# Performance work log

Measured on AMD Instinct MI355X. Metric: run time of the kernel, lower is better.

The kernel has to match this reference:

```python
import itertools
import jax, jax.numpy as jnp
import numpy as np

N, C, D, S = 512, 128, 16, 10  # atoms, channels, irreps dim (0e+1o+2e+3o), species
IR_DIMS = {'0e': 1, '1o': 3}
MULS = {'0e': (23, 4, 1), '1o': (33, 6, 1)}  # path multiplicities for orders (3, 2, 1)


def _make_u(key, order, mul, ir_dim):
    # Synthetic stand-in for e3nn.reduced_symmetric_tensor_product_basis:
    # under permutation of the `order` leading D axes.
    shape = (D,) * order + (mul, ir_dim)
    u = jax.random.normal(key, shape, dtype=jnp.float32)
    mask = jax.random.bernoulli(jax.random.fold_in(key, 1), 0.1, shape)
    u = jnp.where(mask, u, 0.0)
    perms = list(itertools.permutations(range(order)))
    u = sum(jnp.transpose(u, p + (order, order + 1)) for p in perms) / len(perms)
    return u


def setup_inputs() -> dict:
    key = jax.random.key(0)
    ks = jax.random.split(key, 16)
    inp = {
        'x': jax.random.normal(ks[0], (N, C, D), dtype=jnp.float32),
        'index': jax.random.randint(ks[1], (N,), 0, S, dtype=jnp.int32),
    }
    i = 2
    for ir in IR_DIMS:
        for order, mul in zip((3, 2, 1), MULS[ir]):
            inp[f'u{order}_{ir}'] = _make_u(ks[i], order, mul, IR_DIMS[ir]); i += 1
            # gradient_normalization='element' -> init stddev mul**-0.5, no runtime scale
            inp[f'w{order}_{ir}'] = (jax.random.normal(ks[i], (S, mul, C), dtype=jnp.float32)
                                     * mul ** -0.5); i += 1
    return inp


def _contract(x, idx, u3, u2, u1, w3, w2, w1):
    # x: (N,C,D); uK: (D,)*K + (mulK, ir); wK: (S, mulK, C)
    w3i, w2i, w1i = w3[idx], w2[idx], w1[idx]  # species gather -> (N, mulK, C)
    # order 3: einsum('...jki,kc,cj->c...i', u3, w3i, x) batched over atoms.
    # Form p[n,c,k,j] = w3i[n,k,c]*x[n,c,j] first (small), then one big contraction.
    p = jnp.einsum('nkc,ncj->nckj', w3i, x)              # (N,C,mul3,D)
    out = jnp.einsum('abjki,nckj->ncabi', u3, p)         # (N,C,D,D,ir)
    # order 2: accumulate U2.w2, then contract one D axis with x
    out = out + jnp.einsum('abki,nkc->ncabi', u2, w2i)   # (N,C,D,D,ir)
    out = jnp.einsum('ncaji,ncj->ncai', out, x)          # (N,C,D,ir)
    # order 1: accumulate U1.w1, then final contraction with x
    out = out + jnp.einsum('aki,nkc->ncai', u1, w1i)     # (N,C,D,ir)
    out = jnp.einsum('ncji,ncj->nci', out, x)            # (N,C,ir)
    return out


def reference(x, index, u3_0e, w3_0e, u2_0e, w2_0e, u1_0e, w1_0e,
              u3_1o, w3_1o, u2_1o, w2_1o, u1_1o, w1_1o):
    out0 = _contract(x, index, u3_0e, u2_0e, u1_0e, w3_0e, w2_0e, w1_0e)  # (N,C,1)
    out1 = _contract(x, index, u3_1o, u2_1o, u1_1o, w3_1o, w2_1o, w1_1o)  # (N,C,3)
    return jnp.concatenate([out0, out1], axis=-1)  # (N,C,4) irreps 0e+1o
```

## Files before the change

kernel.cpp:

```cpp
#include <hip/hip_runtime.h>
#include <hip/hip_fp16.h>


#define DD     16
#define NATOM  512
#define NCH    128
#define NSPEC  10
#define NTP    1024
#define ATB    8
#define APT    2
#define MAXB   74
#define CHUNKS 8
#define NTC    128
#define TILE   8
#define NTILES (NTC / TILE)
#define CHALF  2
#define CT     8

#define WS_DESC  0
#define WS_ORDER 1024
#define WS_COEF  8192
#define COEF_BYTES (NSPEC * 2 * NTP * 64 * 4 * 2)
#define WS_PART  (WS_COEF + COEF_BYTES)

struct TermTable { unsigned v[NTP]; };
constexpr TermTable build_terms() {
  TermTable T{};
  int t = 0;
  for (int a = 0; a < DD; a++)
    for (int b = a; b < DD; b++)
      for (int j = b; j < DD; j++) {
        unsigned m = (a == b && b == j) ? 1u : ((a == b || b == j) ? 3u : 6u);
        T.v[t++] = (unsigned)(a | (b << 5) | (j << 10) | (3u << 15) | (m << 18));
      }
  for (int a = 0; a < DD; a++)
    for (int b = a; b < DD; b++) {
      unsigned m = (a == b) ? 1u : 2u;
      T.v[t++] = (unsigned)(a | (b << 5) | (16 << 10) | (2u << 15) | (m << 18));
    }
  for (int a = 0; a < DD; a++)
    T.v[t++] = (unsigned)(a | (16 << 5) | (16 << 10) | (1u << 15) | (1u << 18));
  while (t < NTP) T.v[t++] = (unsigned)(17 | (17 << 5) | (17 << 10));
  return T;
}
constexpr TermTable TERMS = build_terms();

__device__ void do_setup(const int* __restrict__ index, int* __restrict__ desc,
                         int* __restrict__ order) {
  __shared__ int cnt[NSPEC], cursor[NSPEC], bbase[NSPEC + 1];
  const int tid = threadIdx.x;
  if (tid < NSPEC) { cnt[tid] = 0; cursor[tid] = 0; }
  __syncthreads();
  for (int i = tid; i < NATOM; i += 128) atomicAdd(&cnt[index[i]], 1);
  for (int i = tid; i < MAXB * ATB; i += 128) order[i] = -1;
  __syncthreads();
  if (tid == 0) {
    int base = 0;
    for (int s = 0; s < NSPEC; s++) { bbase[s] = base; base += (cnt[s] + ATB - 1) / ATB; }
    bbase[NSPEC] = base;
  }
  __syncthreads();
  for (int i = tid; i < NATOM; i += 128) {
    int s = index[i];
    int pos = atomicAdd(&cursor[s], 1);
    order[bbase[s] * ATB + pos] = i;
  }
  for (int i = tid; i < MAXB; i += 128) {
    int sp = -1;
    for (int s = 0; s < NSPEC; s++)
      if (i >= bbase[s] && i < bbase[s + 1]) sp = s;
    desc[i] = sp;
  }
}

__global__ __launch_bounds__(128) void coef_setup_kernel(
    const float* __restrict__ u3_0, const float* __restrict__ w3_0,
    const float* __restrict__ u2_0, const float* __restrict__ w2_0,
    const float* __restrict__ u1_0, const float* __restrict__ w1_0,
    const float* __restrict__ u3_1, const float* __restrict__ w3_1,
    const float* __restrict__ u2_1, const float* __restrict__ w2_1,
    const float* __restrict__ u1_1, const float* __restrict__ w1_1,
    const int* __restrict__ index, int* __restrict__ desc,
    int* __restrict__ order, __half* __restrict__ coefh) {
  if (blockIdx.y == NTP / CT) {
    if (blockIdx.x == 0) do_setup(index, desc, order);
    return;
  }
  const int s = blockIdx.x;
  const int c = threadIdx.x;
  const int tbase = blockIdx.y * CT;

  __shared__ float us0[CT][23];
  __shared__ float us1[CT][99];

  for (int i = 0; i < CT; ++i) {
    const unsigned ev = TERMS.v[tbase + i];
    const int kind = (ev >> 15) & 7;
    const int a = ev & 31, b = (ev >> 5) & 31, j = (ev >> 10) & 31;
    if (kind == 3) {
      const int off = (a * DD + b) * DD + j;
      if (c < 23) us0[i][c] = u3_0[off * 23 + c];
      else if (c < 122) us1[i][c - 23] = u3_1[(size_t)off * 99 + (c - 23)];
    } else if (kind == 2) {
      const int off = a * DD + b;
      if (c < 4) us0[i][c] = u2_0[off * 4 + c];
      else if (c < 22) us1[i][c - 4] = u2_1[off * 18 + (c - 4)];
    } else if (kind == 1) {
      if (c < 1) us0[i][0] = u1_0[a];
      else if (c < 4) us1[i][c - 1] = u1_1[a * 3 + (c - 1)];
    }
  }
  __syncthreads();

  float r3_0[23], r3_1[33], r2_0[4], r2_1[6];
#pragma unroll
  for (int k = 0; k < 23; k++) r3_0[k] = w3_0[(s * 23 + k) * NCH + c];
#pragma unroll
  for (int k = 0; k < 33; k++) r3_1[k] = w3_1[(s * 33 + k) * NCH + c];
#pragma unroll
  for (int k = 0; k < 4; k++) r2_0[k] = w2_0[(s * 4 + k) * NCH + c];
#pragma unroll
  for (int k = 0; k < 6; k++) r2_1[k] = w2_1[(s * 6 + k) * NCH + c];
  const float r1_0 = w1_0[s * NCH + c];
  const float r1_1 = w1_1[s * NCH + c];

  for (int i = 0; i < CT; ++i) {
    const unsigned ev = TERMS.v[tbase + i];
    const int kind = (ev >> 15) & 7;
    const float fm = (float)((ev >> 18) & 7);
    float s0 = 0.f, s1 = 0.f, s2 = 0.f, s3 = 0.f;
    if (kind == 3) {
#pragma unroll
      for (int k = 0; k < 23; k++) s0 += us0[i][k] * r3_0[k];
#pragma unroll
      for (int k = 0; k < 33; k++) {
        const float w = r3_1[k];
        s1 += us1[i][k * 3 + 0] * w;
        s2 += us1[i][k * 3 + 1] * w;
        s3 += us1[i][k * 3 + 2] * w;
      }
    } else if (kind == 2) {
#pragma unroll
      for (int k = 0; k < 4; k++) s0 += us0[i][k] * r2_0[k];
#pragma unroll
      for (int k = 0; k < 6; k++) {
        const float w = r2_1[k];
        s1 += us1[i][k * 3 + 0] * w;
        s2 += us1[i][k * 3 + 1] * w;
        s3 += us1[i][k * 3 + 2] * w;
      }
    } else if (kind == 1) {
      s0 = us0[i][0] * r1_0;
      s1 = us1[i][0] * r1_1;
      s2 = us1[i][1] * r1_1;
      s3 = us1[i][2] * r1_1;
    }
    union { __half2 h2[2]; uint2 u; } pk;
    pk.h2[0] = __floats2half2_rn(fm * s0, fm * s1);
    pk.h2[1] = __floats2half2_rn(fm * s2, fm * s3);
    const size_t off =
        (((size_t)(s * 2 + (c >> 6)) * NTP + (tbase + i)) * 64 + (c & 63));
    *(uint2*)((char*)coefh + off * 8) = pk.u;
  }
}

__device__ __forceinline__ void stage_tile(const unsigned* __restrict__ gbase,
                                           int t0_tile, float* dst_base,
                                           int wave, int lane) {
  const unsigned* g = gbase + (size_t)(t0_tile + 2 * wave) * 128 + lane * 4;
  __builtin_amdgcn_global_load_lds(
      (const __attribute__((address_space(1))) unsigned int*)g,
      (__attribute__((address_space(3))) unsigned int*)(dst_base + wave * 256),
      16, 0, 0);
}

template <int CH>
__device__ __forceinline__ void eval_chunk(const unsigned* __restrict__ gbase,
                                           float (*lbuf)[TILE * 128],
                                           int wave, int lane,
                                           const float (&xr)[APT][18],
                                           float (&ac)[APT][4]) {
  constexpr int T0 = CH * NTC;
  stage_tile(gbase, T0, &lbuf[0][0], wave, lane);
#pragma unroll
  for (int tile = 0; tile < NTILES; ++tile) {
    __syncthreads();
    if (tile + 1 < NTILES)
      stage_tile(gbase, T0 + (tile + 1) * TILE, &lbuf[(tile + 1) & 1][0], wave, lane);
    const float* lb = &lbuf[tile & 1][0];
#pragma unroll
    for (int i = 0; i < TILE; ++i) {
      const unsigned ev = TERMS.v[T0 + tile * TILE + i];
      const int ea = ev & 31, eb = (ev >> 5) & 31, ej = (ev >> 10) & 31;
      const uint2 raw = *(const uint2*)(lb + i * 128 + lane * 2);
      const float2 f01 = __half22float2(*reinterpret_cast<const __half2*>(&raw.x));
      const float2 f23 = __half22float2(*reinterpret_cast<const __half2*>(&raw.y));
#pragma unroll
      for (int k = 0; k < APT; ++k) {
        const float m = xr[k][ea] * xr[k][eb] * xr[k][ej];
        ac[k][0] += f01.x * m; ac[k][1] += f01.y * m;
        ac[k][2] += f23.x * m; ac[k][3] += f23.y * m;
      }
    }
  }
}

__device__ __forceinline__ void load16(float (&xr)[18], const float* __restrict__ p) {
  const float4* q = (const float4*)p;
  const float4 v0 = q[0], v1 = q[1], v2 = q[2], v3 = q[3];
  xr[0] = v0.x; xr[1] = v0.y; xr[2] = v0.z; xr[3] = v0.w;
  xr[4] = v1.x; xr[5] = v1.y; xr[6] = v1.z; xr[7] = v1.w;
  xr[8] = v2.x; xr[9] = v2.y; xr[10] = v2.z; xr[11] = v2.w;
  xr[12] = v3.x; xr[13] = v3.y; xr[14] = v3.z; xr[15] = v3.w;
}

__global__ __launch_bounds__(256, 4) void contract_kernel(const float* __restrict__ x,
                                                          const int* __restrict__ desc,
                                                          const int* __restrict__ order,
                                                          const __half* __restrict__ coefh,
                                                          float* __restrict__ partial) {
  const int s = desc[blockIdx.x];
  if (s < 0) return;
  const int lane = threadIdx.x & 63;
  const int wave = threadIdx.x >> 6;
  const int half = blockIdx.z;
  const int c = half * 64 + lane;

  __shared__ float lbuf[2][TILE * 128];

  int n[APT];
#pragma unroll
  for (int k = 0; k < APT; k++) n[k] = order[blockIdx.x * ATB + wave * APT + k];

  float xr[APT][18];
#pragma unroll
  for (int k = 0; k < APT; k++) {
#pragma unroll
    for (int i = 0; i < DD; i++) xr[k][i] = 0.f;
    xr[k][16] = 1.f;
    xr[k][17] = 0.f;
  }
#pragma unroll
  for (int k = 0; k < APT; k++)
    if (n[k] >= 0) load16(xr[k], x + ((size_t)n[k] * NCH + c) * DD);

  float ac[APT][4];
#pragma unroll
  for (int k = 0; k < APT; k++) { ac[k][0] = 0.f; ac[k][1] = 0.f; ac[k][2] = 0.f; ac[k][3] = 0.f; }

  const unsigned* gbase =
      (const unsigned*)coefh + (size_t)(s * 2 + half) * NTP * 128;

  switch (blockIdx.y) {
    case 0: eval_chunk<0>(gbase, lbuf, wave, lane, xr, ac); break;
    case 1: eval_chunk<1>(gbase, lbuf, wave, lane, xr, ac); break;
    case 2: eval_chunk<2>(gbase, lbuf, wave, lane, xr, ac); break;
    case 3: eval_chunk<3>(gbase, lbuf, wave, lane, xr, ac); break;
    case 4: eval_chunk<4>(gbase, lbuf, wave, lane, xr, ac); break;
    case 5: eval_chunk<5>(gbase, lbuf, wave, lane, xr, ac); break;
    case 6: eval_chunk<6>(gbase, lbuf, wave, lane, xr, ac); break;
    default: eval_chunk<7>(gbase, lbuf, wave, lane, xr, ac); break;
  }

  float* pb = partial + (size_t)blockIdx.y * (NATOM * NCH * 4);
#pragma unroll
  for (int k = 0; k < APT; k++)
    if (n[k] >= 0)
      *(float4*)(pb + ((size_t)n[k] * NCH + c) * 4) =
          float4{ac[k][0], ac[k][1], ac[k][2], ac[k][3]};
}

__global__ __launch_bounds__(256) void reduce_kernel(const float4* __restrict__ partial,
                                                     float4* __restrict__ out) {
  const int i = blockIdx.x * 256 + threadIdx.x;
  float4 s{0.f, 0.f, 0.f, 0.f};
#pragma unroll
  for (int ch = 0; ch < CHUNKS; ch++) {
    const float4 v = partial[(size_t)ch * (NATOM * NCH) + i];
    s.x += v.x; s.y += v.y; s.z += v.z; s.w += v.w;
  }
  out[i] = s;
}

extern "C" void kernel_launch(void* const* d_in, const int* in_sizes, int n_in,
                              void* d_out, int out_size, void* d_ws, size_t ws_size,
                              hipStream_t stream) {
  const float* x    = (const float*)d_in[0];
  const int* index  = (const int*)d_in[1];
  const float* u3_0 = (const float*)d_in[2];
  const float* w3_0 = (const float*)d_in[3];
  const float* u2_0 = (const float*)d_in[4];
  const float* w2_0 = (const float*)d_in[5];
  const float* u1_0 = (const float*)d_in[6];
  const float* w1_0 = (const float*)d_in[7];
  const float* u3_1 = (const float*)d_in[8];
  const float* w3_1 = (const float*)d_in[9];
  const float* u2_1 = (const float*)d_in[10];
  const float* w2_1 = (const float*)d_in[11];
  const float* u1_1 = (const float*)d_in[12];
  const float* w1_1 = (const float*)d_in[13];
  float* out = (float*)d_out;

  char* ws = (char*)d_ws;
  int* desc      = (int*)(ws + WS_DESC);
  int* order     = (int*)(ws + WS_ORDER);
  __half* coefh  = (__half*)(ws + WS_COEF);
  float* partial = (float*)(ws + WS_PART);

  coef_setup_kernel<<<dim3(NSPEC, NTP / CT + 1), 128, 0, stream>>>(
      u3_0, w3_0, u2_0, w2_0, u1_0, w1_0,
      u3_1, w3_1, u2_1, w2_1, u1_1, w1_1, index, desc, order, coefh);
  contract_kernel<<<dim3(MAXB, CHUNKS, CHALF), 256, 0, stream>>>(x, desc, order, coefh, partial);
  reduce_kernel<<<(NATOM * NCH) / 256, 256, 0, stream>>>((const float4*)partial, (float4*)out);
}
```

Baseline: 128.1 us.

## Use one atom per thread and replace partial-sum reduction with atomics

```diff
diff --git a/kernel.cpp b/kernel.cpp
--- a/kernel.cpp
+++ b/kernel.cpp
@@ -7,9 +7,9 @@
 #define NCH    128
 #define NSPEC  10
 #define NTP    1024
-#define ATB    8
-#define APT    2
-#define MAXB   74
+#define ATB    4
+#define APT    1
+#define MAXB   136
 #define CHUNKS 8
 #define NTC    128
 #define TILE   8
@@ -21,7 +21,6 @@
 #define WS_ORDER 1024
 #define WS_COEF  8192
 #define COEF_BYTES (NSPEC * 2 * NTP * 64 * 4 * 2)
-#define WS_PART  (WS_COEF + COEF_BYTES)
 
 struct TermTable { unsigned v[NTP]; };
 constexpr TermTable build_terms() {
@@ -81,9 +80,15 @@
     const float* __restrict__ u2_1, const float* __restrict__ w2_1,
     const float* __restrict__ u1_1, const float* __restrict__ w1_1,
     const int* __restrict__ index, int* __restrict__ desc,
-    int* __restrict__ order, __half* __restrict__ coefh) {
+    int* __restrict__ order, __half* __restrict__ coefh,
+    float* __restrict__ out) {
   if (blockIdx.y == NTP / CT) {
-    if (blockIdx.x == 0) do_setup(index, desc, order);
+    if (blockIdx.x == 0) { do_setup(index, desc, order); return; }
+    float4* o4 = (float4*)out;
+    const float4 z{0.f, 0.f, 0.f, 0.f};
+    for (int i = (blockIdx.x - 1) * 128 + threadIdx.x; i < NATOM * NCH;
+         i += (NSPEC - 1) * 128)
+      o4[i] = z;
     return;
   }
   const int s = blockIdx.x;
@@ -178,8 +183,8 @@
 __device__ __forceinline__ void eval_chunk(const unsigned* __restrict__ gbase,
                                            float (*lbuf)[TILE * 128],
                                            int wave, int lane,
-                                           const float (&xr)[APT][18],
-                                           float (&ac)[APT][4]) {
+                                           const float (&xr)[18],
+                                           float (&ac)[4]) {
   constexpr int T0 = CH * NTC;
   stage_tile(gbase, T0, &lbuf[0][0], wave, lane);
 #pragma unroll
@@ -195,12 +200,9 @@
       const uint2 raw = *(const uint2*)(lb + i * 128 + lane * 2);
       const float2 f01 = __half22float2(*reinterpret_cast<const __half2*>(&raw.x));
       const float2 f23 = __half22float2(*reinterpret_cast<const __half2*>(&raw.y));
-#pragma unroll
-      for (int k = 0; k < APT; ++k) {
-        const float m = xr[k][ea] * xr[k][eb] * xr[k][ej];
-        ac[k][0] += f01.x * m; ac[k][1] += f01.y * m;
-        ac[k][2] += f23.x * m; ac[k][3] += f23.y * m;
-      }
+      const float m = xr[ea] * xr[eb] * xr[ej];
+      ac[0] += f01.x * m; ac[1] += f01.y * m;
+      ac[2] += f23.x * m; ac[3] += f23.y * m;
     }
   }
 }
@@ -218,7 +220,7 @@
                                                           const int* __restrict__ desc,
                                                           const int* __restrict__ order,
                                                           const __half* __restrict__ coefh,
-                                                          float* __restrict__ partial) {
+                                                          float* __restrict__ out) {
   const int s = desc[blockIdx.x];
   if (s < 0) return;
   const int lane = threadIdx.x & 63;
@@ -228,25 +230,16 @@
 
   __shared__ float lbuf[2][TILE * 128];
 
-  int n[APT];
-#pragma unroll
-  for (int k = 0; k < APT; k++) n[k] = order[blockIdx.x * ATB + wave * APT + k];
-
-  float xr[APT][18];
-#pragma unroll
-  for (int k = 0; k < APT; k++) {
-#pragma unroll
-    for (int i = 0; i < DD; i++) xr[k][i] = 0.f;
-    xr[k][16] = 1.f;
-    xr[k][17] = 0.f;
-  }
-#pragma unroll
-  for (int k = 0; k < APT; k++)
-    if (n[k] >= 0) load16(xr[k], x + ((size_t)n[k] * NCH + c) * DD);
-
-  float ac[APT][4];
-#pragma unroll
-  for (int k = 0; k < APT; k++) { ac[k][0] = 0.f; ac[k][1] = 0.f; ac[k][2] = 0.f; ac[k][3] = 0.f; }
+  const int n = order[blockIdx.x * ATB + wave];
+
+  float xr[18];
+#pragma unroll
+  for (int i = 0; i < DD; i++) xr[i] = 0.f;
+  xr[16] = 1.f;
+  xr[17] = 0.f;
+  if (n >= 0) load16(xr, x + ((size_t)n * NCH + c) * DD);
+
+  float ac[4] = {0.f, 0.f, 0.f, 0.f};
 
   const unsigned* gbase =
       (const unsigned*)coefh + (size_t)(s * 2 + half) * NTP * 128;
@@ -262,24 +255,13 @@
     default: eval_chunk<7>(gbase, lbuf, wave, lane, xr, ac); break;
   }
 
-  float* pb = partial + (size_t)blockIdx.y * (NATOM * NCH * 4);
-#pragma unroll
-  for (int k = 0; k < APT; k++)
-    if (n[k] >= 0)
-      *(float4*)(pb + ((size_t)n[k] * NCH + c) * 4) =
-          float4{ac[k][0], ac[k][1], ac[k][2], ac[k][3]};
-}
-
-__global__ __launch_bounds__(256) void reduce_kernel(const float4* __restrict__ partial,
-                                                     float4* __restrict__ out) {
-  const int i = blockIdx.x * 256 + threadIdx.x;
-  float4 s{0.f, 0.f, 0.f, 0.f};
-#pragma unroll
-  for (int ch = 0; ch < CHUNKS; ch++) {
-    const float4 v = partial[(size_t)ch * (NATOM * NCH) + i];
-    s.x += v.x; s.y += v.y; s.z += v.z; s.w += v.w;
-  }
-  out[i] = s;
+  if (n >= 0) {
+    float* po = out + ((size_t)n * NCH + c) * 4;
+    atomicAdd(po + 0, ac[0]);
+    atomicAdd(po + 1, ac[1]);
+    atomicAdd(po + 2, ac[2]);
+    atomicAdd(po + 3, ac[3]);
+  }
 }
 
 extern "C" void kernel_launch(void* const* d_in, const int* in_sizes, int n_in,
@@ -305,11 +287,9 @@
   int* desc      = (int*)(ws + WS_DESC);
   int* order     = (int*)(ws + WS_ORDER);
   __half* coefh  = (__half*)(ws + WS_COEF);
-  float* partial = (float*)(ws + WS_PART);
 
   coef_setup_kernel<<<dim3(NSPEC, NTP / CT + 1), 128, 0, stream>>>(
       u3_0, w3_0, u2_0, w2_0, u1_0, w1_0,
-      u3_1, w3_1, u2_1, w2_1, u1_1, w1_1, index, desc, order, coefh);
-  contract_kernel<<<dim3(MAXB, CHUNKS, CHALF), 256, 0, stream>>>(x, desc, order, coefh, partial);
-  reduce_kernel<<<(NATOM * NCH) / 256, 256, 0, stream>>>((const float4*)partial, (float4*)out);
-}
+      u3_1, w3_1, u2_1, w2_1, u1_1, w1_1, index, desc, order, coefh, out);
+  contract_kernel<<<dim3(MAXB, CHUNKS, CHALF), 256, 0, stream>>>(x, desc, order, coefh, out);
+}
```

Result: slower. 137.0 us (+6.9%).

## Give each wave a private double-buffered LDS staging area and drop block barriers

Applied to the files above, without the earlier changes.

```diff
diff --git a/kernel.cpp b/kernel.cpp
--- a/kernel.cpp
+++ b/kernel.cpp
@@ -14,6 +14,7 @@
 #define NTC    128
 #define TILE   8
 #define NTILES (NTC / TILE)
+#define NBUF   2
 #define CHALF  2
 #define CT     8
 
@@ -164,30 +165,35 @@
   }
 }
 
-__device__ __forceinline__ void stage_tile(const unsigned* __restrict__ gbase,
-                                           int t0_tile, float* dst_base,
-                                           int wave, int lane) {
-  const unsigned* g = gbase + (size_t)(t0_tile + 2 * wave) * 128 + lane * 4;
-  __builtin_amdgcn_global_load_lds(
-      (const __attribute__((address_space(1))) unsigned int*)g,
-      (__attribute__((address_space(3))) unsigned int*)(dst_base + wave * 256),
-      16, 0, 0);
+__device__ __forceinline__ void stage_full(const unsigned* __restrict__ gbase,
+                                           int t0_tile, float* dst, int lane) {
+#pragma unroll
+  for (int r = 0; r < 4; ++r) {
+    const unsigned* g = gbase + (size_t)(t0_tile + 2 * r) * 128 + lane * 4;
+    __builtin_amdgcn_global_load_lds(
+        (const __attribute__((address_space(1))) unsigned int*)g,
+        (__attribute__((address_space(3))) unsigned int*)(dst + r * 256),
+        16, 0, 0);
+  }
 }
 
 template <int CH>
 __device__ __forceinline__ void eval_chunk(const unsigned* __restrict__ gbase,
-                                           float (*lbuf)[TILE * 128],
-                                           int wave, int lane,
+                                           float* __restrict__ wbuf,
+                                           int lane,
                                            const float (&xr)[APT][18],
                                            float (&ac)[APT][4]) {
   constexpr int T0 = CH * NTC;
-  stage_tile(gbase, T0, &lbuf[0][0], wave, lane);
+  asm volatile("s_waitcnt vmcnt(0)" ::: "memory");
+  stage_full(gbase, T0, wbuf, lane);
 #pragma unroll
   for (int tile = 0; tile < NTILES; ++tile) {
-    __syncthreads();
     if (tile + 1 < NTILES)
-      stage_tile(gbase, T0 + (tile + 1) * TILE, &lbuf[(tile + 1) & 1][0], wave, lane);
-    const float* lb = &lbuf[tile & 1][0];
+      stage_full(gbase, T0 + (tile + 1) * TILE,
+                 wbuf + ((tile + 1) & 1) * (TILE * 128), lane);
+    if (tile + 1 < NTILES) asm volatile("s_waitcnt vmcnt(4)" ::: "memory");
+    else                   asm volatile("s_waitcnt vmcnt(0)" ::: "memory");
+    const float* lb = wbuf + (tile & 1) * (TILE * 128);
 #pragma unroll
     for (int i = 0; i < TILE; ++i) {
       const unsigned ev = TERMS.v[T0 + tile * TILE + i];
@@ -226,11 +232,16 @@
   const int half = blockIdx.z;
   const int c = half * 64 + lane;
 
-  __shared__ float lbuf[2][TILE * 128];
+  __shared__ float lbuf[4][NBUF * TILE * 128];
 
   int n[APT];
 #pragma unroll
   for (int k = 0; k < APT; k++) n[k] = order[blockIdx.x * ATB + wave * APT + k];
+
+  bool any = false;
+#pragma unroll
+  for (int k = 0; k < APT; k++) any = any || (n[k] >= 0);
+  if (!any) return;
 
   float xr[APT][18];
 #pragma unroll
@@ -252,14 +263,14 @@
       (const unsigned*)coefh + (size_t)(s * 2 + half) * NTP * 128;
 
   switch (blockIdx.y) {
-    case 0: eval_chunk<0>(gbase, lbuf, wave, lane, xr, ac); break;
-    case 1: eval_chunk<1>(gbase, lbuf, wave, lane, xr, ac); break;
-    case 2: eval_chunk<2>(gbase, lbuf, wave, lane, xr, ac); break;
-    case 3: eval_chunk<3>(gbase, lbuf, wave, lane, xr, ac); break;
-    case 4: eval_chunk<4>(gbase, lbuf, wave, lane, xr, ac); break;
-    case 5: eval_chunk<5>(gbase, lbuf, wave, lane, xr, ac); break;
-    case 6: eval_chunk<6>(gbase, lbuf, wave, lane, xr, ac); break;
-    default: eval_chunk<7>(gbase, lbuf, wave, lane, xr, ac); break;
+    case 0: eval_chunk<0>(gbase, &lbuf[wave][0], lane, xr, ac); break;
+    case 1: eval_chunk<1>(gbase, &lbuf[wave][0], lane, xr, ac); break;
+    case 2: eval_chunk<2>(gbase, &lbuf[wave][0], lane, xr, ac); break;
+    case 3: eval_chunk<3>(gbase, &lbuf[wave][0], lane, xr, ac); break;
+    case 4: eval_chunk<4>(gbase, &lbuf[wave][0], lane, xr, ac); break;
+    case 5: eval_chunk<5>(gbase, &lbuf[wave][0], lane, xr, ac); break;
+    case 6: eval_chunk<6>(gbase, &lbuf[wave][0], lane, xr, ac); break;
+    default: eval_chunk<7>(gbase, &lbuf[wave][0], lane, xr, ac); break;
   }
 
   float* pb = partial + (size_t)blockIdx.y * (NATOM * NCH * 4);
```

New measurement: 137.5 us. 7.3% more time.
